# Performance work log

Hardware: AMD Instinct MI355X
Metric: run time of the kernel (lower is better)

The kernel has to match this reference:

```python
import jax, jax.numpy as jnp
import numpy as np

B, N, D, C = 16, 100, 256, 2  # batch, num_nodes, d_model, num_classes


def _make_edge_index(n):
    # torch.combinations(arange(n), r=2).T then cat with reversed rows
    i, j = np.triu_indices(n, k=1)
    src = np.concatenate([i, j])
    dst = np.concatenate([j, i])
    return jnp.asarray(np.stack([src, dst]), dtype=jnp.int32)  # [2, N*(N-1)]


def setup_inputs() -> dict:
    key = jax.random.key(0)
    ks = jax.random.split(key, 10)
    s = 1.0 / np.sqrt(D)
    s2 = 1.0 / np.sqrt(2 * D)
    return {
        "hidden_state": jax.random.normal(ks[0], (B, N, D), jnp.float32),
        "pred_bboxes": jax.random.uniform(ks[1], (B, N, 4), jnp.float32),
        "W1": jax.random.normal(ks[2], (D, D), jnp.float32) * s,
        "b1": jnp.zeros((D,), jnp.float32),
        "W2": jax.random.normal(ks[3], (D, D), jnp.float32) * s,
        "b2": jnp.zeros((D,), jnp.float32),
        "Wl1": jax.random.normal(ks[4], (2 * D, D), jnp.float32) * s2,
        "bl1": jnp.zeros((D,), jnp.float32),
        "Wf": jax.random.normal(ks[5], (D, C), jnp.float32) * s,
        "bf": jnp.zeros((C,), jnp.float32),
        "edge_index": _make_edge_index(N),
    }


def gcn_conv(x, W, b, src, dst, n):
    # PyG GCNConv: add self-loops, symmetric deg^-1/2 normalization,
    # linear transform, scatter-add aggregation at dst, then bias.
    # x: [B, n, D_in]
    xw = x @ W  # [B, n, D_out]
    loop = jnp.arange(n, dtype=src.dtype)
    src_sl = jnp.concatenate([src, loop])
    dst_sl = jnp.concatenate([dst, loop])
    deg = jnp.zeros((n,), xw.dtype).at[dst_sl].add(1.0)
    dis = jax.lax.rsqrt(deg)
    norm = dis[src_sl] * dis[dst_sl]  # [E+n]
    msg = xw[:, src_sl] * norm[None, :, None]  # gather + scale
    out = jnp.zeros_like(xw).at[:, dst_sl].add(msg)  # scatter-add
    return out + b


def reference(hidden_state, pred_bboxes, W1, b1, W2, b2, Wl1, bl1, Wf, bf, edge_index):
    src, dst = edge_index[0], edge_index[1]
    n = hidden_state.shape[1]
    x = jax.nn.relu(gcn_conv(hidden_state, W1, b1, src, dst, n))
    x = jax.nn.relu(gcn_conv(x, W2, b2, src, dst, n))
    # pairwise edge readout
    xpair = jnp.concatenate([x[:, src], x[:, dst]], axis=-1)  # [B, E, 2D]
    xpair = jax.nn.relu(xpair @ Wl1 + bl1)
    xfin = xpair @ Wf + bf  # [B, E, C]
    probs = jax.nn.log_softmax(xfin, axis=-1)
    bbox_pairs = jnp.concatenate([pred_bboxes[:, src], pred_bboxes[:, dst]], axis=-1)
    return probs, bbox_pairs
```

## Files before the change

### kernel.cpp

```cpp
#include <hip/hip_runtime.h>
#include <hip/hip_bf16.h>


#define BB 16
#define NN 100
#define DD 256
#define EE 9900
#define CHUNK 1238

typedef float f32x4 __attribute__((ext_vector_type(4)));
typedef float f32x2 __attribute__((ext_vector_type(2)));

__device__ __forceinline__ f32x4 ldg_nt4(const float* p) {
    return __builtin_nontemporal_load(reinterpret_cast<const f32x4*>(p));
}
__device__ __forceinline__ f32x4 ld4(const float* p) {
    return *reinterpret_cast<const f32x4*>(p);
}
__device__ __forceinline__ void stg_nt4(float* p, f32x4 v) {
    __builtin_nontemporal_store(v, reinterpret_cast<f32x4*>(p));
}

__global__ __launch_bounds__(256) void k_mlp(
    const float* __restrict__ x,
    const float* __restrict__ bboxes,
    const int*   __restrict__ edge,
    const float* __restrict__ W1, const float* __restrict__ b1,
    const float* __restrict__ W2, const float* __restrict__ b2,
    const float* __restrict__ Wl1, const float* __restrict__ bl1,
    const float* __restrict__ Wf,
    float* __restrict__ ws,
    float* __restrict__ out)
{
    const int b  = blockIdx.x >> 3;
    const int g  = blockIdx.x & 7;
    const int t  = threadIdx.x;
    const int c4 = t & 63;
    const int kq = t >> 6;

    __shared__ __align__(16) float sX[DD];
    __shared__ __align__(16) float sY[DD];
    __shared__ __align__(16) f32x4 sPf[256];
    __shared__ float sL0[8], sL1[8];

    {
        const float* xp = x + ((size_t)b * NN + kq * 25) * DD + c4 * 4;
        f32x4 a = {0.f, 0.f, 0.f, 0.f};
        #pragma unroll
        for (int n = 0; n < 25; ++n)
            a += ld4(xp + (size_t)n * DD);
        sPf[kq * 64 + c4] = a;
    }

    {
        const int e0 = g * CHUNK;
        const int e1 = min(e0 + CHUNK, EE);
        float* boutf = out + (size_t)BB * EE * 2;
        for (int e = e0 + t; e < e1; e += 256) {
            const int s  = edge[e];
            const int d2 = edge[EE + e];
            const size_t idx = (size_t)b * EE + e;
            f32x4 bs = ld4(bboxes + (size_t)(b * NN + s) * 4);
            f32x4 bd = ld4(bboxes + (size_t)(b * NN + d2) * 4);
            stg_nt4(boutf + idx * 8, bs);
            stg_nt4(boutf + idx * 8 + 4, bd);
        }
    }
    __syncthreads();
    if (t < 64) {
        f32x4 s = sPf[t] + sPf[64 + t] + sPf[128 + t] + sPf[192 + t];
        ((f32x4*)sX)[t] = s * 0.01f;
    }
    __syncthreads();

    {
        const float* Wp = W1 + (size_t)(kq * 64) * DD + c4 * 4;
        const float* xk = sX + kq * 64;
        f32x4 acc = {0.f, 0.f, 0.f, 0.f};
        #pragma unroll 8
        for (int k = 0; k < 64; ++k)
            acc += xk[k] * ldg_nt4(Wp + (size_t)k * DD);
        __syncthreads();
        sPf[kq * 64 + c4] = acc;
        __syncthreads();
        if (t < 64) {
            f32x4 s = sPf[t] + sPf[64 + t] + sPf[128 + t] + sPf[192 + t]
                    + ld4(b1 + t * 4);
            f32x4 z = {0.f, 0.f, 0.f, 0.f};
            ((f32x4*)sY)[t] = __builtin_elementwise_max(s, z);
        }
        __syncthreads();
    }

    {
        const float* Wp = W2 + (size_t)(kq * 64) * DD + c4 * 4;
        const float* xk = sY + kq * 64;
        f32x4 acc = {0.f, 0.f, 0.f, 0.f};
        #pragma unroll 8
        for (int k = 0; k < 64; ++k)
            acc += xk[k] * ldg_nt4(Wp + (size_t)k * DD);
        __syncthreads();
        sPf[kq * 64 + c4] = acc;
        __syncthreads();
        if (t < 64) {
            f32x4 s = sPf[t] + sPf[64 + t] + sPf[128 + t] + sPf[192 + t]
                    + ld4(b2 + t * 4);
            f32x4 z = {0.f, 0.f, 0.f, 0.f};
            ((f32x4*)sX)[t] = __builtin_elementwise_max(s, z);
        }
        __syncthreads();
    }

    {
        const int c8  = t & 7;
        const int k32 = t >> 3;
        const float* Wp0 = Wl1 + (size_t)(k32 * 8) * DD + g * 32 + c8 * 4;
        const float* Wp1 = Wp0 + (size_t)DD * DD;
        const float* xk = sX + k32 * 8;
        f32x4 acc = {0.f, 0.f, 0.f, 0.f};
        #pragma unroll
        for (int k = 0; k < 8; ++k) {
            f32x4 w = ldg_nt4(Wp0 + (size_t)k * DD) + ldg_nt4(Wp1 + (size_t)k * DD);
            acc += xk[k] * w;
        }
        __syncthreads();
        sPf[k32 * 8 + c8] = acc;
        __syncthreads();
        if (t < 8) {
            f32x4 s = {0.f, 0.f, 0.f, 0.f};
            #pragma unroll
            for (int q = 0; q < 32; ++q) s += sPf[q * 8 + t];
            const int c0 = g * 32 + t * 4;
            s += ld4(bl1 + c0);
            f32x4 z = {0.f, 0.f, 0.f, 0.f};
            f32x4 h = __builtin_elementwise_max(s, z);
            sL0[t] = h.x * Wf[(c0 + 0) * 2] + h.y * Wf[(c0 + 1) * 2]
                   + h.z * Wf[(c0 + 2) * 2] + h.w * Wf[(c0 + 3) * 2];
            sL1[t] = h.x * Wf[(c0 + 0) * 2 + 1] + h.y * Wf[(c0 + 1) * 2 + 1]
                   + h.z * Wf[(c0 + 2) * 2 + 1] + h.w * Wf[(c0 + 3) * 2 + 1];
        }
        __syncthreads();
        if (t == 0) {
            float l0 = 0.f, l1 = 0.f;
            #pragma unroll
            for (int i = 0; i < 8; ++i) { l0 += sL0[i]; l1 += sL1[i]; }
            ws[(b * 8 + g) * 2 + 0] = l0;
            ws[(b * 8 + g) * 2 + 1] = l1;
        }
    }
}

__global__ __launch_bounds__(256) void k_probs(
    const float* __restrict__ ws,
    const float* __restrict__ bf,
    float* __restrict__ out)
{
    const int b = blockIdx.y;
    const int e = blockIdx.x * 256 + threadIdx.x;

    __shared__ float sp0, sp1;
    if (threadIdx.x == 0) {
        float L0 = bf[0], L1 = bf[1];
        #pragma unroll
        for (int q = 0; q < 8; ++q) {
            L0 += ws[(b * 8 + q) * 2 + 0];
            L1 += ws[(b * 8 + q) * 2 + 1];
        }
        float m  = fmaxf(L0, L1);
        float ls = logf(expf(L0 - m) + expf(L1 - m));
        sp0 = L0 - m - ls;
        sp1 = L1 - m - ls;
    }
    __syncthreads();

    if (e < EE) {
        f32x2 p = {sp0, sp1};
        __builtin_nontemporal_store(
            p, reinterpret_cast<f32x2*>(out) + (size_t)b * EE + e);
    }
}

extern "C" void kernel_launch(void* const* d_in, const int* in_sizes, int n_in,
                              void* d_out, int out_size, void* d_ws, size_t ws_size,
                              hipStream_t stream) {
    const float* hidden  = (const float*)d_in[0];
    const float* bboxes  = (const float*)d_in[1];
    const float* W1      = (const float*)d_in[2];
    const float* b1      = (const float*)d_in[3];
    const float* W2      = (const float*)d_in[4];
    const float* b2      = (const float*)d_in[5];
    const float* Wl1     = (const float*)d_in[6];
    const float* bl1     = (const float*)d_in[7];
    const float* Wf      = (const float*)d_in[8];
    const float* bf      = (const float*)d_in[9];
    const int*   edge    = (const int*)d_in[10];

    float* ws  = (float*)d_ws;
    float* out = (float*)d_out;

    k_mlp<<<BB * 8, 256, 0, stream>>>(hidden, bboxes, edge,
                                      W1, b1, W2, b2, Wl1, bl1, Wf,
                                      ws, out);

    dim3 og((EE + 255) / 256, BB);
    k_probs<<<og, 256, 0, stream>>>(ws, bf, out);
}
```

Baseline: 16.86 us.

## Double blocks per batch and batch weight loads for more memory parallelism

Each batch is now split across 16 blocks instead of 8, which halves the bbox gather chunk and the Wl1 column slice per block and adds a two-stage shared-memory reduction. The W1/W2 matvec loops load 16 weight rows into registers before their FMAs, and each block starts at a rotated k-chunk so concurrent blocks touch different weight rows. The hidden-state mean is also split into batched loads. The aim is more bytes in flight and more occupied CUs on this latency-bound kernel, at the cost of the redundant W1/W2 matvec running in twice as many blocks and extra register pressure.

```diff
diff --git a/kernel.cpp b/kernel.cpp
--- a/kernel.cpp
+++ b/kernel.cpp
@@ -6,7 +6,8 @@
 #define NN 100
 #define DD 256
 #define EE 9900
-#define CHUNK 1238
+#define GG 16
+#define CHUNK 619
 
 typedef float f32x4 __attribute__((ext_vector_type(4)));
 typedef float f32x2 __attribute__((ext_vector_type(2)));
@@ -32,23 +33,36 @@
     float* __restrict__ ws,
     float* __restrict__ out)
 {
-    const int b  = blockIdx.x >> 3;
-    const int g  = blockIdx.x & 7;
+    const int b  = blockIdx.x >> 4;
+    const int g  = blockIdx.x & 15;
     const int t  = threadIdx.x;
     const int c4 = t & 63;
     const int kq = t >> 6;
+    const int ph = blockIdx.x & 3;
 
     __shared__ __align__(16) float sX[DD];
     __shared__ __align__(16) float sY[DD];
     __shared__ __align__(16) f32x4 sPf[256];
-    __shared__ float sL0[8], sL1[8];
+    __shared__ float sR[32 * 4];
+    __shared__ float sL0[4], sL1[4];
 
     {
         const float* xp = x + ((size_t)b * NN + kq * 25) * DD + c4 * 4;
         f32x4 a = {0.f, 0.f, 0.f, 0.f};
-        #pragma unroll
-        for (int n = 0; n < 25; ++n)
-            a += ld4(xp + (size_t)n * DD);
+        {
+            f32x4 v[13];
+            #pragma unroll
+            for (int i = 0; i < 13; ++i) v[i] = ld4(xp + (size_t)i * DD);
+            #pragma unroll
+            for (int i = 0; i < 13; ++i) a += v[i];
+        }
+        {
+            f32x4 v[12];
+            #pragma unroll
+            for (int i = 0; i < 12; ++i) v[i] = ld4(xp + (size_t)(13 + i) * DD);
+            #pragma unroll
+            for (int i = 0; i < 12; ++i) a += v[i];
+        }
         sPf[kq * 64 + c4] = a;
     }
 
@@ -77,9 +91,17 @@
         const float* Wp = W1 + (size_t)(kq * 64) * DD + c4 * 4;
         const float* xk = sX + kq * 64;
         f32x4 acc = {0.f, 0.f, 0.f, 0.f};
-        #pragma unroll 8
-        for (int k = 0; k < 64; ++k)
-            acc += xk[k] * ldg_nt4(Wp + (size_t)k * DD);
+        #pragma unroll
+        for (int cc = 0; cc < 4; ++cc) {
+            const int kb = ((ph + cc) & 3) * 16;
+            f32x4 w[16];
+            #pragma unroll
+            for (int i = 0; i < 16; ++i)
+                w[i] = ldg_nt4(Wp + (size_t)(kb + i) * DD);
+            #pragma unroll
+            for (int i = 0; i < 16; ++i)
+                acc += xk[kb + i] * w[i];
+        }
         __syncthreads();
         sPf[kq * 64 + c4] = acc;
         __syncthreads();
@@ -96,9 +118,17 @@
         const float* Wp = W2 + (size_t)(kq * 64) * DD + c4 * 4;
         const float* xk = sY + kq * 64;
         f32x4 acc = {0.f, 0.f, 0.f, 0.f};
-        #pragma unroll 8
-        for (int k = 0; k < 64; ++k)
-            acc += xk[k] * ldg_nt4(Wp + (size_t)k * DD);
+        #pragma unroll
+        for (int cc = 0; cc < 4; ++cc) {
+            const int kb = ((ph + cc) & 3) * 16;
+            f32x4 w[16];
+            #pragma unroll
+            for (int i = 0; i < 16; ++i)
+                w[i] = ldg_nt4(Wp + (size_t)(kb + i) * DD);
+            #pragma unroll
+            for (int i = 0; i < 16; ++i)
+                acc += xk[kb + i] * w[i];
+        }
         __syncthreads();
         sPf[kq * 64 + c4] = acc;
         __syncthreads();
@@ -112,25 +142,38 @@
     }
 
     {
-        const int c8  = t & 7;
-        const int k32 = t >> 3;
-        const float* Wp0 = Wl1 + (size_t)(k32 * 8) * DD + g * 32 + c8 * 4;
+        const int c  = t & 3;
+        const int kg = t >> 2;
+        const float* Wp0 = Wl1 + (size_t)(kg * 4) * DD + g * 16 + c * 4;
         const float* Wp1 = Wp0 + (size_t)DD * DD;
-        const float* xk = sX + k32 * 8;
+        const float* xk = sX + kg * 4;
+        f32x4 w0[4], w1[4];
+        #pragma unroll
+        for (int i = 0; i < 4; ++i) w0[i] = ldg_nt4(Wp0 + (size_t)i * DD);
+        #pragma unroll
+        for (int i = 0; i < 4; ++i) w1[i] = ldg_nt4(Wp1 + (size_t)i * DD);
         f32x4 acc = {0.f, 0.f, 0.f, 0.f};
         #pragma unroll
-        for (int k = 0; k < 8; ++k) {
-            f32x4 w = ldg_nt4(Wp0 + (size_t)k * DD) + ldg_nt4(Wp1 + (size_t)k * DD);
-            acc += xk[k] * w;
-        }
-        __syncthreads();
-        sPf[k32 * 8 + c8] = acc;
-        __syncthreads();
-        if (t < 8) {
+        for (int i = 0; i < 4; ++i)
+            acc += xk[i] * (w0[i] + w1[i]);
+        __syncthreads();
+        sPf[kg * 4 + c] = acc;
+        __syncthreads();
+        if (t < 32) {
+            const int c2 = t & 3, r = t >> 2;
             f32x4 s = {0.f, 0.f, 0.f, 0.f};
             #pragma unroll
-            for (int q = 0; q < 32; ++q) s += sPf[q * 8 + t];
-            const int c0 = g * 32 + t * 4;
+            for (int j = 0; j < 8; ++j)
+                s += sPf[(r * 8 + j) * 4 + c2];
+            *(f32x4*)&sR[t * 4] = s;
+        }
+        __syncthreads();
+        if (t < 4) {
+            f32x4 s = {0.f, 0.f, 0.f, 0.f};
+            #pragma unroll
+            for (int r = 0; r < 8; ++r)
+                s += *(const f32x4*)&sR[(r * 4 + t) * 4];
+            const int c0 = g * 16 + t * 4;
             s += ld4(bl1 + c0);
             f32x4 z = {0.f, 0.f, 0.f, 0.f};
             f32x4 h = __builtin_elementwise_max(s, z);
@@ -141,11 +184,10 @@
         }
         __syncthreads();
         if (t == 0) {
-            float l0 = 0.f, l1 = 0.f;
-            #pragma unroll
-            for (int i = 0; i < 8; ++i) { l0 += sL0[i]; l1 += sL1[i]; }
-            ws[(b * 8 + g) * 2 + 0] = l0;
-            ws[(b * 8 + g) * 2 + 1] = l1;
+            float l0 = sL0[0] + sL0[1] + sL0[2] + sL0[3];
+            float l1 = sL1[0] + sL1[1] + sL1[2] + sL1[3];
+            ws[(b * GG + g) * 2 + 0] = l0;
+            ws[(b * GG + g) * 2 + 1] = l1;
         }
     }
 }
@@ -162,9 +204,9 @@
     if (threadIdx.x == 0) {
         float L0 = bf[0], L1 = bf[1];
         #pragma unroll
-        for (int q = 0; q < 8; ++q) {
-            L0 += ws[(b * 8 + q) * 2 + 0];
-            L1 += ws[(b * 8 + q) * 2 + 1];
+        for (int q = 0; q < GG; ++q) {
+            L0 += ws[(b * GG + q) * 2 + 0];
+            L1 += ws[(b * GG + q) * 2 + 1];
         }
         float m  = fmaxf(L0, L1);
         float ls = logf(expf(L0 - m) + expf(L1 - m));
@@ -198,9 +240,9 @@
     float* ws  = (float*)d_ws;
     float* out = (float*)d_out;
 
-    k_mlp<<<BB * 8, 256, 0, stream>>>(hidden, bboxes, edge,
-                                      W1, b1, W2, b2, Wl1, bl1, Wf,
-                                      ws, out);
+    k_mlp<<<BB * GG, 256, 0, stream>>>(hidden, bboxes, edge,
+                                       W1, b1, W2, b2, Wl1, bl1, Wf,
+                                       ws, out);
 
     dim3 og((EE + 255) / 256, BB);
     k_probs<<<og, 256, 0, stream>>>(ws, bf, out);
```

Measured after the change: 16.87 us. About the same (+0.1%).
